# Optimization experiments

Hardware: AMD Instinct MI355X
Metric: run time of the kernel (lower is better)

## Reference

```python
import jax, jax.numpy as jnp
import numpy as np

D_MODEL = 1024
N_HEAD = 16
HEAD_DIM = D_MODEL // N_HEAD


def setup_inputs() -> dict:
    key = jax.random.key(0)
    ks = jax.random.split(key, 11)
    B, S = 2, 2048
    scale = 1.0 / np.sqrt(D_MODEL)
    inp = {
        'q': jax.random.normal(ks[0], (B, S, D_MODEL), dtype=jnp.float32),
        'k': jax.random.normal(ks[1], (B, S, D_MODEL), dtype=jnp.float32),
        'v': jax.random.normal(ks[2], (B, S, D_MODEL), dtype=jnp.float32),
        'Wq': jax.random.normal(ks[3], (D_MODEL, D_MODEL), dtype=jnp.float32) * scale,
        'bq': jnp.zeros((D_MODEL,), dtype=jnp.float32),
        'Wk': jax.random.normal(ks[4], (D_MODEL, D_MODEL), dtype=jnp.float32) * scale,
        'bk': jnp.zeros((D_MODEL,), dtype=jnp.float32),
        'Wv': jax.random.normal(ks[5], (D_MODEL, D_MODEL), dtype=jnp.float32) * scale,
        'bv': jnp.zeros((D_MODEL,), dtype=jnp.float32),
        'Wo': jax.random.normal(ks[6], (D_MODEL, D_MODEL), dtype=jnp.float32) * scale,
        'bo': jnp.zeros((D_MODEL,), dtype=jnp.float32),
    }
    return inp


def _split_heads(x):
    # [B, S, D] -> [B, H, S, Dh]
    B, S, _ = x.shape
    return x.reshape(B, S, N_HEAD, HEAD_DIM).transpose(0, 2, 1, 3)


def reference(q, k, v, Wq, bq, Wk, bk, Wv, bv, Wo, bo):
    B, S, _ = q.shape
    qh = _split_heads(q @ Wq + bq)  # [B,H,S,Dh]
    kh = _split_heads(k @ Wk + bk)
    vh = _split_heads(v @ Wv + bv)
    inv_sqrt_d = jnp.asarray(1.0 / np.sqrt(HEAD_DIM), dtype=q.dtype)
    scores = jnp.einsum('bhqd,bhkd->bhqk', qh, kh) * inv_sqrt_d  # [B,H,S,S]
    attn = jax.nn.softmax(scores, axis=-1)
    out = jnp.einsum('bhqk,bhkd->bhqd', attn, vh)  # [B,H,S,Dh]
    out = out.transpose(0, 2, 1, 3).reshape(B, S, D_MODEL)
    return out @ Wo + bo
```

## Files before the change

kernel.cpp:

```cpp
#include <hip/hip_runtime.h>
#include <cstdint>
#include <cstddef>

#define D_MODEL 1024
#define NHEAD 16
#define HDIM 64
#define BATCH 2
#define SEQ 2048
#define MROWS (BATCH*SEQ)

typedef _Float16 f16;
typedef _Float16 f16x2 __attribute__((ext_vector_type(2)));
typedef _Float16 f16x4 __attribute__((ext_vector_type(4)));
typedef _Float16 f16x8 __attribute__((ext_vector_type(8)));
typedef float f32x4 __attribute__((ext_vector_type(4)));
typedef __fp16 fp16x2_raw __attribute__((ext_vector_type(2)));

__device__ __forceinline__ f16x2 cvt_pk(float a, float b) {
  fp16x2_raw t = __builtin_amdgcn_cvt_pkrtz(a, b);
  return __builtin_bit_cast(f16x2, t);
}

__device__ __forceinline__ float fast_exp2(float x) {
  return __builtin_amdgcn_exp2f(x);
}

#define QSCALE 0.18033688011112042f
#define CSHIFT 6.0f

__device__ __forceinline__ void gload_lds16(const void* gsrc, void* ldst) {
  __builtin_amdgcn_global_load_lds(
      (__attribute__((address_space(1))) void*)gsrc,
      (__attribute__((address_space(3))) void*)ldst,
      16, 0, 0);
}

__global__ __launch_bounds__(256) void cast3_kernel(
    const float* __restrict__ q, const float* __restrict__ k,
    const float* __restrict__ v, f16* __restrict__ Xf) {
  const int z = blockIdx.y;
  const float* in = (z == 0) ? q : (z == 1) ? k : v;
  f16* out = Xf + (size_t)z * MROWS * D_MODEL;
  int i = (blockIdx.x * 256 + threadIdx.x) * 8;
  const float4* p = (const float4*)(in + i);
  float4 a = p[0], b = p[1];
  f16x8 o = { (f16)a.x,(f16)a.y,(f16)a.z,(f16)a.w,
              (f16)b.x,(f16)b.y,(f16)b.z,(f16)b.w };
  *(f16x8*)(out + i) = o;
}

__global__ __launch_bounds__(256) void transpose4_kernel(
    const float* __restrict__ W0, const float* __restrict__ W1,
    const float* __restrict__ W2, const float* __restrict__ W3,
    f16* __restrict__ T0, f16* __restrict__ T1,
    f16* __restrict__ T2, f16* __restrict__ T3) {
  const int z = blockIdx.z;
  const float* W = (z == 0) ? W0 : (z == 1) ? W1 : (z == 2) ? W2 : W3;
  f16* Wt = (z == 0) ? T0 : (z == 1) ? T1 : (z == 2) ? T2 : T3;
  __shared__ float tile[32][33];
  int n0 = blockIdx.x * 32, k0 = blockIdx.y * 32;
  int tx = threadIdx.x, ty = threadIdx.y;
  #pragma unroll
  for (int j = 0; j < 32; j += 8)
    tile[ty + j][tx] = W[(size_t)(k0 + ty + j) * D_MODEL + n0 + tx];
  __syncthreads();
  #pragma unroll
  for (int j = 0; j < 32; j += 8)
    Wt[(size_t)(n0 + ty + j) * D_MODEL + k0 + tx] = (f16)tile[tx][ty + j];
}

__global__ __launch_bounds__(256, 3) void gemm_qkv(
    const f16* __restrict__ Xf,
    const f16* __restrict__ Wtq, const f16* __restrict__ Wtk, const f16* __restrict__ Wtv,
    const float* __restrict__ bq, const float* __restrict__ bk, const float* __restrict__ bv,
    f16* __restrict__ Qh, f16* __restrict__ Kf, f16* __restrict__ Vf) {
  __shared__ __align__(16) f16 As[128 * 64];
  __shared__ __align__(16) f16 Bs[128 * 64];
  const int id = blockIdx.x;
  const int xcd = id & 7;
  const int s5 = id >> 3;
  const int bn_i = s5 & 7;
  const int t5 = xcd * 12 + (s5 >> 3);
  const int z = t5 >> 5;
  const int bm_i = t5 & 31;
  const int bm = bm_i * 128, bn = bn_i * 128;
  const f16* A  = Xf + (size_t)z * MROWS * D_MODEL + (size_t)bm * 1024;
  const f16* Bt = ((z == 0) ? Wtq : (z == 1) ? Wtk : Wtv) + (size_t)bn * 1024;
  const float* bias = (z == 0) ? bq : (z == 1) ? bk : bv;
  const int tid = threadIdx.x, wave = tid >> 6, lane = tid & 63;
  const int lr = lane & 15, lq = lane >> 4, sw = lr & 7;
  const int wm = (wave >> 1) * 64, wn = (wave & 1) * 64;
  const int srow = lane >> 3;
  const int scs  = (lane & 7) ^ srow;
  const f16* Ag = A  + (size_t)(wave * 32 + srow) * 1024 + scs * 8;
  const f16* Bg = Bt + (size_t)(wave * 32 + srow) * 1024 + scs * 8;

  f32x4 acc[4][4];
  #pragma unroll
  for (int i = 0; i < 4; i++)
    #pragma unroll
    for (int j = 0; j < 4; j++) acc[i][j] = (f32x4){0.f, 0.f, 0.f, 0.f};

  for (int k0 = 0; k0 < 1024; k0 += 64) {
    __syncthreads();
    #pragma unroll
    for (int g = 0; g < 4; g++) {
      gload_lds16(Ag + (size_t)g * 8 * 1024 + k0, As + wave * 2048 + g * 512);
      gload_lds16(Bg + (size_t)g * 8 * 1024 + k0, Bs + wave * 2048 + g * 512);
    }
    __syncthreads();
    #pragma unroll
    for (int t = 0; t < 2; t++) {
      f16x8 af[4], bf[4];
      #pragma unroll
      for (int m = 0; m < 4; m++)
        af[m] = *(const f16x8*)(As + (size_t)(wm + m * 16 + lr) * 64 + (((t * 4 + lq) ^ sw) * 8));
      #pragma unroll
      for (int j = 0; j < 4; j++)
        bf[j] = *(const f16x8*)(Bs + (size_t)(wn + j * 16 + lr) * 64 + (((t * 4 + lq) ^ sw) * 8));
      #pragma unroll
      for (int m = 0; m < 4; m++)
        #pragma unroll
        for (int j = 0; j < 4; j++)
          acc[m][j] = __builtin_amdgcn_mfma_f32_16x16x32_f16(af[m], bf[j], acc[m][j], 0, 0, 0);
    }
  }

  #pragma unroll
  for (int j = 0; j < 4; j++) {
    const int col = bn + wn + j * 16 + lr;
    const float bj = bias[col];
    const int hh = col >> 6, d = col & 63;
    #pragma unroll
    for (int m = 0; m < 4; m++) {
      #pragma unroll
      for (int r = 0; r < 4; r++) {
        const int row = bm + wm + m * 16 + lq * 4 + r;
        float val = acc[m][j][r] + bj;
        if (z == 0) val *= QSCALE;
        const int b = row >> 11, s = row & 2047;
        const size_t bh = (size_t)b * NHEAD + hh;
        const int tile = s >> 6;
        if (z == 0) {
          Qh[(bh * SEQ + s) * HDIM + d] = (f16)val;
        } else if (z == 1) {
          const int kk = s & 63;
          const int f = ((kk >> 4) << 1) | (d >> 5);
          const int ln = ((d >> 3) & 3) * 16 + (kk & 15);
          Kf[((bh * 32 + tile) * 8 + f) * 512 + ln * 8 + (d & 7)] = (f16)val;
        } else {
          const int kp = (((s >> 4) & 1) << 5) | (((s >> 2) & 3) << 3)
                       | (((s >> 5) & 1) << 2) | (s & 3);
          const int f = ((d >> 4) << 1) | (kp >> 5);
          const int ln = ((kp >> 3) & 3) * 16 + (d & 15);
          Vf[((bh * 32 + tile) * 8 + f) * 512 + ln * 8 + (kp & 7)] = (f16)val;
        }
      }
    }
  }
}

__global__ __launch_bounds__(256, 4) void gemm_o(
    const f16* __restrict__ AO, const f16* __restrict__ Wto,
    const float* __restrict__ bo, float* __restrict__ out) {
  __shared__ __align__(16) f16 As[64 * 64];
  __shared__ __align__(16) f16 Bs[128 * 64];
  const int id = blockIdx.x;
  const int xcd = id & 7;
  const int s5 = id >> 3;
  const int bn_i = s5 & 7;
  const int bm_i = xcd * 8 + (s5 >> 3);
  const int bm = bm_i * 64, bn = bn_i * 128;
  const int tid = threadIdx.x, wave = tid >> 6, lane = tid & 63;
  const int lr = lane & 15, lq = lane >> 4, sw = lr & 7;
  const int wm = (wave >> 1) * 32, wn = (wave & 1) * 64;
  const int srow = lane >> 3;
  const int scs  = (lane & 7) ^ srow;
  const f16* Ag = AO  + (size_t)(bm + wave * 16 + srow) * 1024 + scs * 8;
  const f16* Bg = Wto + (size_t)(bn + wave * 32 + srow) * 1024 + scs * 8;

  f32x4 acc[2][4];
  #pragma unroll
  for (int i = 0; i < 2; i++)
    #pragma unroll
    for (int j = 0; j < 4; j++) acc[i][j] = (f32x4){0.f, 0.f, 0.f, 0.f};

  for (int k0 = 0; k0 < 1024; k0 += 64) {
    __syncthreads();
    #pragma unroll
    for (int g = 0; g < 2; g++)
      gload_lds16(Ag + (size_t)g * 8 * 1024 + k0, As + wave * 1024 + g * 512);
    #pragma unroll
    for (int g = 0; g < 4; g++)
      gload_lds16(Bg + (size_t)g * 8 * 1024 + k0, Bs + wave * 2048 + g * 512);
    __syncthreads();
    #pragma unroll
    for (int t = 0; t < 2; t++) {
      f16x8 af[2], bf[4];
      #pragma unroll
      for (int m = 0; m < 2; m++)
        af[m] = *(const f16x8*)(As + (size_t)(wm + m * 16 + lr) * 64 + (((t * 4 + lq) ^ sw) * 8));
      #pragma unroll
      for (int j = 0; j < 4; j++)
        bf[j] = *(const f16x8*)(Bs + (size_t)(wn + j * 16 + lr) * 64 + (((t * 4 + lq) ^ sw) * 8));
      #pragma unroll
      for (int m = 0; m < 2; m++)
        #pragma unroll
        for (int j = 0; j < 4; j++)
          acc[m][j] = __builtin_amdgcn_mfma_f32_16x16x32_f16(af[m], bf[j], acc[m][j], 0, 0, 0);
    }
  }
  #pragma unroll
  for (int j = 0; j < 4; j++) {
    const int col = bn + wn + j * 16 + lr;
    const float bj = bo[col];
    #pragma unroll
    for (int m = 0; m < 2; m++)
      #pragma unroll
      for (int r = 0; r < 4; r++) {
        const int row = bm + wm + m * 16 + lq * 4 + r;
        out[(size_t)row * D_MODEL + col] = acc[m][j][r] + bj;
      }
  }
}

__global__ __launch_bounds__(256, 2) void flash_kernel(
    const f16* __restrict__ Qh, const f16* __restrict__ Kf,
    const f16* __restrict__ Vf, f16* __restrict__ AO) {
  const int id = blockIdx.x;
  const int xcd = id & 7;
  const int s6 = id >> 3;
  const int q_i = s6 & 15;
  const int hl = xcd * 4 + (s6 >> 4);
  const int h = hl & 15, b = hl >> 4;
  const int tid = threadIdx.x, wave = tid >> 6, lane = tid & 63;
  const int lr = lane & 15, lq = lane >> 4;
  const size_t bh = (size_t)b * NHEAD + h;
  const f16* Qb = Qh + bh * SEQ * HDIM;
  const f16* Kb = Kf + bh * 32 * 4096 + lane * 8;
  const f16* Vb = Vf + bh * 32 * 4096 + lane * 8;
  const int q0 = q_i * 128 + wave * 32;

  f16x8 aq[2][2];
  #pragma unroll
  for (int m = 0; m < 2; m++)
    #pragma unroll
    for (int t = 0; t < 2; t++)
      aq[m][t] = *(const f16x8*)(Qb + (size_t)(q0 + m * 16 + lr) * HDIM + t * 32 + lq * 8);

  f32x4 oacc[2][4], ls[2];
  #pragma unroll
  for (int m = 0; m < 2; m++) {
    ls[m] = (f32x4){0.f, 0.f, 0.f, 0.f};
    #pragma unroll
    for (int j = 0; j < 4; j++) oacc[m][j] = (f32x4){0.f, 0.f, 0.f, 0.f};
  }
  const f32x4 mC = {-CSHIFT, -CSHIFT, -CSHIFT, -CSHIFT};
  const f16x8 ones = {(f16)1, (f16)1, (f16)1, (f16)1, (f16)1, (f16)1, (f16)1, (f16)1};

  #define FITER(KC, KN, it, PF, QKW, PVW)                                      \
    do {                                                                       \
      f16x8 vv[8];                                                             \
      _Pragma("unroll")                                                        \
      for (int f = 0; f < 8; f++)                                              \
        vv[f] = *(const f16x8*)(Vb + ((size_t)(it) * 8 + f) * 512);            \
      if (PF) {                                                                \
        _Pragma("unroll")                                                      \
        for (int f = 0; f < 8; f++)                                            \
          KN[f] = *(const f16x8*)(Kb + ((size_t)((it) + 1) * 8 + f) * 512);    \
      }                                                                        \
      __builtin_amdgcn_sched_barrier(0);                                       \
      asm volatile("s_waitcnt vmcnt(" #QKW ")" ::: "memory");                  \
      __builtin_amdgcn_sched_barrier(0);                                       \
      f32x4 sc[4][2];                                                          \
      _Pragma("unroll")                                                        \
      for (int t = 0; t < 2; t++)                                              \
        _Pragma("unroll")                                                      \
        for (int j = 0; j < 4; j++)                                            \
          _Pragma("unroll")                                                    \
          for (int m = 0; m < 2; m++)                                          \
            sc[j][m] = __builtin_amdgcn_mfma_f32_16x16x32_f16(                 \
                KC[j * 2 + t], aq[m][t], (t == 0) ? mC : sc[j][m], 0, 0, 0);   \
      f16x8 ap[2][2];                                                          \
      _Pragma("unroll")                                                        \
      for (int m = 0; m < 2; m++)                                              \
        _Pragma("unroll")                                                      \
        for (int t = 0; t < 2; t++) {                                          \
          union { f16x8 v; f16x2 h2[4]; } u;                                   \
          const f32x4 lo = sc[t][m], hi = sc[t + 2][m];                        \
          u.h2[0] = cvt_pk(fast_exp2(lo[0]), fast_exp2(lo[1]));                \
          u.h2[1] = cvt_pk(fast_exp2(lo[2]), fast_exp2(lo[3]));                \
          u.h2[2] = cvt_pk(fast_exp2(hi[0]), fast_exp2(hi[1]));                \
          u.h2[3] = cvt_pk(fast_exp2(hi[2]), fast_exp2(hi[3]));                \
          ap[m][t] = u.v;                                                      \
        }                                                                      \
      asm volatile("s_waitcnt vmcnt(" #PVW ")" ::: "memory");                  \
      __builtin_amdgcn_sched_barrier(0);                                       \
      _Pragma("unroll")                                                        \
      for (int t = 0; t < 2; t++) {                                            \
        _Pragma("unroll")                                                      \
        for (int j = 0; j < 4; j++)                                            \
          _Pragma("unroll")                                                    \
          for (int m = 0; m < 2; m++)                                          \
            oacc[m][j] = __builtin_amdgcn_mfma_f32_16x16x32_f16(               \
                ap[m][t], vv[j * 2 + t], oacc[m][j], 0, 0, 0);                 \
        _Pragma("unroll")                                                      \
        for (int m = 0; m < 2; m++)                                            \
          ls[m] = __builtin_amdgcn_mfma_f32_16x16x32_f16(                      \
              ap[m][t], ones, ls[m], 0, 0, 0);                                 \
      }                                                                        \
    } while (0)

  f16x8 kA[8], kB[8];
  #pragma unroll
  for (int f = 0; f < 8; f++)
    kA[f] = *(const f16x8*)(Kb + (size_t)f * 512);

  for (int it2 = 0; it2 < 15; it2++) {
    FITER(kA, kB, it2 * 2,     1, 16, 8);
    FITER(kB, kA, it2 * 2 + 1, 1, 16, 8);
  }
  FITER(kA, kB, 30, 1, 16, 8);
  FITER(kB, kA, 31, 0, 8, 0);
  #undef FITER

  #pragma unroll
  for (int m = 0; m < 2; m++)
    #pragma unroll
    for (int r = 0; r < 4; r++) {
      const float inv = 1.0f / ls[m][r];
      const int row = q0 + m * 16 + lq * 4 + r;
      #pragma unroll
      for (int j = 0; j < 4; j++) {
        const int col = h * HDIM + j * 16 + lr;
        AO[((size_t)b * SEQ + row) * D_MODEL + col] = (f16)(oacc[m][j][r] * inv);
      }
    }
}

extern "C" void kernel_launch(void* const* d_in, const int* in_sizes, int n_in,
                              void* d_out, int out_size, void* d_ws, size_t ws_size,
                              hipStream_t stream) {
  const float* q  = (const float*)d_in[0];
  const float* k  = (const float*)d_in[1];
  const float* v  = (const float*)d_in[2];
  const float* Wq = (const float*)d_in[3];
  const float* bq = (const float*)d_in[4];
  const float* Wk = (const float*)d_in[5];
  const float* bk = (const float*)d_in[6];
  const float* Wv = (const float*)d_in[7];
  const float* bv = (const float*)d_in[8];
  const float* Wo = (const float*)d_in[9];
  const float* bo = (const float*)d_in[10];
  float* out = (float*)d_out;

  char* ws = (char*)d_ws;
  f16* Wt_q = (f16*)(ws + ((size_t)0  << 20));
  f16* Wt_k = (f16*)(ws + ((size_t)2  << 20));
  f16* Wt_v = (f16*)(ws + ((size_t)4  << 20));
  f16* Wt_o = (f16*)(ws + ((size_t)6  << 20));
  f16* Xf   = (f16*)(ws + ((size_t)8  << 20));
  f16* Qh_  = (f16*)(ws + ((size_t)32 << 20));
  f16* Kf_  = (f16*)(ws + ((size_t)40 << 20));
  f16* Vf_  = (f16*)(ws + ((size_t)48 << 20));
  f16* AO   = Xf;

  transpose4_kernel<<<dim3(32, 32, 4), dim3(32, 8), 0, stream>>>(
      Wq, Wk, Wv, Wo, Wt_q, Wt_k, Wt_v, Wt_o);

  cast3_kernel<<<dim3(2048, 3), 256, 0, stream>>>(q, k, v, Xf);

  gemm_qkv<<<768, 256, 0, stream>>>(
      Xf, Wt_q, Wt_k, Wt_v, bq, bk, bv, Qh_, Kf_, Vf_);

  flash_kernel<<<512, 256, 0, stream>>>(Qh_, Kf_, Vf_, AO);

  gemm_o<<<512, 256, 0, stream>>>(AO, Wt_o, bo, out);
}
```

Baseline: 220.4 us.

## Share K tiles across waves via LDS double buffer with direct global-to-LDS loads

Each wave used to load the full K tile for every key block into its own registers, so the four waves of a block fetched the same data four times. Now each wave issues two direct global-to-LDS loads into a double-buffered shared K tile, then reads its fragments from LDS before the QK MFMAs. A wait-all plus block barrier at the end of each iteration keeps the buffers consistent. This cuts redundant global/L2 traffic and frees about 64 VGPRs, at the cost of LDS reads and one block-wide barrier per iteration.

```diff
diff --git a/kernel.cpp b/kernel.cpp
--- a/kernel.cpp
+++ b/kernel.cpp
@@ -227,6 +227,7 @@
 __global__ __launch_bounds__(256, 2) void flash_kernel(
     const f16* __restrict__ Qh, const f16* __restrict__ Kf,
     const f16* __restrict__ Vf, f16* __restrict__ AO) {
+  __shared__ __align__(16) f16 Ks[2][8 * 512];
   const int id = blockIdx.x;
   const int xcd = id & 7;
   const int s6 = id >> 3;
@@ -258,29 +259,33 @@
   const f32x4 mC = {-CSHIFT, -CSHIFT, -CSHIFT, -CSHIFT};
   const f16x8 ones = {(f16)1, (f16)1, (f16)1, (f16)1, (f16)1, (f16)1, (f16)1, (f16)1};
 
-  #define FITER(KC, KN, it, PF, QKW, PVW)                                      \
+  #define FITER(it, CUR, PF, PVW)                                              \
     do {                                                                       \
       f16x8 vv[8];                                                             \
       _Pragma("unroll")                                                        \
       for (int f = 0; f < 8; f++)                                              \
         vv[f] = *(const f16x8*)(Vb + ((size_t)(it) * 8 + f) * 512);            \
       if (PF) {                                                                \
-        _Pragma("unroll")                                                      \
-        for (int f = 0; f < 8; f++)                                            \
-          KN[f] = *(const f16x8*)(Kb + ((size_t)((it) + 1) * 8 + f) * 512);    \
+        gload_lds16(Kb + ((size_t)((it) + 1) * 8 + 2 * wave) * 512,            \
+                    &Ks[(CUR) ^ 1][(2 * wave) * 512]);                         \
+        gload_lds16(Kb + ((size_t)((it) + 1) * 8 + 2 * wave + 1) * 512,        \
+                    &Ks[(CUR) ^ 1][(2 * wave + 1) * 512]);                     \
       }                                                                        \
-      __builtin_amdgcn_sched_barrier(0);                                       \
-      asm volatile("s_waitcnt vmcnt(" #QKW ")" ::: "memory");                  \
       __builtin_amdgcn_sched_barrier(0);                                       \
       f32x4 sc[4][2];                                                          \
       _Pragma("unroll")                                                        \
-      for (int t = 0; t < 2; t++)                                              \
+      for (int t = 0; t < 2; t++) {                                            \
+        f16x8 bk[4];                                                           \
+        _Pragma("unroll")                                                      \
+        for (int j = 0; j < 4; j++)                                            \
+          bk[j] = *(const f16x8*)(&Ks[CUR][(j * 2 + t) * 512 + lane * 8]);     \
         _Pragma("unroll")                                                      \
         for (int j = 0; j < 4; j++)                                            \
           _Pragma("unroll")                                                    \
           for (int m = 0; m < 2; m++)                                          \
             sc[j][m] = __builtin_amdgcn_mfma_f32_16x16x32_f16(                 \
-                KC[j * 2 + t], aq[m][t], (t == 0) ? mC : sc[j][m], 0, 0, 0);   \
+                bk[j], aq[m][t], (t == 0) ? mC : sc[j][m], 0, 0, 0);           \
+      }                                                                        \
       f16x8 ap[2][2];                                                          \
       _Pragma("unroll")                                                        \
       for (int m = 0; m < 2; m++)                                              \
@@ -309,19 +314,23 @@
           ls[m] = __builtin_amdgcn_mfma_f32_16x16x32_f16(                      \
               ap[m][t], ones, ls[m], 0, 0, 0);                                 \
       }                                                                        \
+      if (PF) {                                                                \
+        asm volatile("s_waitcnt vmcnt(0)" ::: "memory");                       \
+        __builtin_amdgcn_s_barrier();                                          \
+        __builtin_amdgcn_sched_barrier(0);                                     \
+      }                                                                        \
     } while (0)
 
-  f16x8 kA[8], kB[8];
-  #pragma unroll
-  for (int f = 0; f < 8; f++)
-    kA[f] = *(const f16x8*)(Kb + (size_t)f * 512);
+  gload_lds16(Kb + (size_t)(2 * wave) * 512, &Ks[0][(2 * wave) * 512]);
+  gload_lds16(Kb + (size_t)(2 * wave + 1) * 512, &Ks[0][(2 * wave + 1) * 512]);
+  __syncthreads();
 
   for (int it2 = 0; it2 < 15; it2++) {
-    FITER(kA, kB, it2 * 2,     1, 16, 8);
-    FITER(kB, kA, it2 * 2 + 1, 1, 16, 8);
-  }
-  FITER(kA, kB, 30, 1, 16, 8);
-  FITER(kB, kA, 31, 0, 8, 0);
+    FITER(it2 * 2,     0, 1, 2);
+    FITER(it2 * 2 + 1, 1, 1, 2);
+  }
+  FITER(30, 0, 1, 2);
+  FITER(31, 1, 0, 0);
   #undef FITER
 
   #pragma unroll
```

After: 205.4 us. 6.8% less time.
